# Kernel tuning notes

Measured on AMD Instinct MI355X. Metric: run time of the kernel, lower is better.

## Reference

```python
import jax, jax.numpy as jnp
import numpy as np

N = 100000      # nodes
E = 1600000     # edges (avg degree 16)
DIN = 32        # input feature dim
H = 16          # nhidden
DEPTH = 4       # number of SAGEConv layers


def setup_inputs() -> dict:
    key = jax.random.key(0)
    ks = jax.random.split(key, 16)
    s = 0.1
    inp = {
        "x": jax.random.normal(ks[0], (N, DIN), jnp.float32),
        "edge_index": jax.random.randint(ks[1], (2, E), 0, N, dtype=jnp.int64),
        # SAGEConv layer 0: in=DIN -> out=H. lin_l has bias, lin_r has no bias (PyG default).
        "Wl0": jax.random.normal(ks[2], (H, DIN), jnp.float32) * s,
        "bl0": jnp.zeros((H,), jnp.float32),
        "Wr0": jax.random.normal(ks[3], (H, DIN), jnp.float32) * s,
        # SAGEConv layers 1..3: in=H -> out=H, stacked.
        "Wls": jax.random.normal(ks[4], (DEPTH - 1, H, H), jnp.float32) * s,
        "bls": jnp.zeros((DEPTH - 1, H), jnp.float32),
        "Wrs": jax.random.normal(ks[5], (DEPTH - 1, H, H), jnp.float32) * s,
        # lin_out MLP: [H, 2H, 2H, 1] with acts [silu, silu, None], no batch norm.
        "W1": jax.random.normal(ks[6], (2 * H, H), jnp.float32) * s,
        "b1": jnp.zeros((2 * H,), jnp.float32),
        "W2": jax.random.normal(ks[7], (2 * H, 2 * H), jnp.float32) * s,
        "b2": jnp.zeros((2 * H,), jnp.float32),
        "W3": jax.random.normal(ks[8], (1, 2 * H), jnp.float32) * s,
        "b3": jnp.zeros((1,), jnp.float32),
    }
    return inp


def reference(x, edge_index, Wl0, bl0, Wr0, Wls, bls, Wrs, W1, b1, W2, b2, W3, b3):
    src = edge_index[0]  # message source (x_j)
    dst = edge_index[1]  # aggregation target (x_i)

    def sage(h, Wl, bl, Wr):
        # sum-aggregate neighbor features, then lin_l(agg) + lin_r(h)
        agg = jax.ops.segment_sum(h[src], dst, num_segments=N)  # [N, d]
        return agg @ Wl.T + bl + h @ Wr.T

    x = jax.nn.silu(sage(x, Wl0, bl0, Wr0))
    for i in range(DEPTH - 1):
        x = jax.nn.silu(sage(x, Wls[i], bls[i], Wrs[i]))

    out = jax.nn.silu(x @ W1.T + b1)
    out = jax.nn.silu(out @ W2.T + b2)
    out = out @ W3.T + b3  # [N, 1]
    return out
```

## Files before the change

kernel.cpp:

```cpp
#include <hip/hip_runtime.h>


#define SH     7
#define BWID   128
#define NBMAX  1024
#define CHUNK  4096
#define EPT    (CHUNK / 256)

__device__ __forceinline__ float silu_f(float v) {
    return v * __builtin_amdgcn_rcpf(1.0f + __expf(-v));
}

__device__ __forceinline__ float bf_lo(unsigned u) { return __uint_as_float(u << 16); }
__device__ __forceinline__ float bf_hi(unsigned u) { return __uint_as_float(u & 0xFFFF0000u); }
__device__ __forceinline__ unsigned short f2bf(float f) {
    unsigned x = __float_as_uint(f);
    unsigned r = x + 0x7FFFu + ((x >> 16) & 1u);
    return (unsigned short)(r >> 16);
}
__device__ __forceinline__ unsigned pack_bf2(float a, float b) {
    return (unsigned)f2bf(a) | ((unsigned)f2bf(b) << 16);
}


__global__ __launch_bounds__(256) void bucket_hist(
    const int* __restrict__ dst, int* __restrict__ bcnt, int ne)
{
    __shared__ int sh[NBMAX];
    const int t = threadIdx.x;
    for (int i = t; i < NBMAX; i += 256) sh[i] = 0;
    __syncthreads();
    const int base = blockIdx.x * CHUNK;
    for (int i = t; i < CHUNK; i += 256) {
        const int e = base + i;
        if (e < ne) atomicAdd(&sh[dst[e] >> SH], 1);
    }
    __syncthreads();
    for (int b = t; b < NBMAX; b += 256) {
        const int c = sh[b];
        if (c) atomicAdd(&bcnt[b], c);
    }
}

__global__ __launch_bounds__(1024) void bucket_scan(
    const int* __restrict__ bcnt, int* __restrict__ bbase,
    int* __restrict__ cursors, int* __restrict__ noff, int nbuck, int n, int ne)
{
    __shared__ int sh[NBMAX];
    const int t = threadIdx.x;
    const int c = (t < nbuck) ? bcnt[t] : 0;
    sh[t] = c;
    __syncthreads();
    int v = c;
    for (int off = 1; off < NBMAX; off <<= 1) {
        const int add = (t >= off) ? sh[t - off] : 0;
        __syncthreads();
        v += add;
        sh[t] = v;
        __syncthreads();
    }
    const int excl = v - c;
    if (t < nbuck) { bbase[t] = excl; cursors[t] = excl; }
    if (t == 0) { bbase[nbuck] = ne; noff[n] = ne; }
}

__global__ __launch_bounds__(256) void bin_kernel(
    const int* __restrict__ src, const int* __restrict__ dst,
    int* __restrict__ cursors, unsigned* __restrict__ binned0, int ne)
{
    __shared__ int   s_hist[NBMAX];
    __shared__ int   s_scan[NBMAX];
    __shared__ int   s_gbase[NBMAX];
    __shared__ int   s_p[256];
    __shared__ uint2 s_items[CHUNK];

    const int t = threadIdx.x;
    const int base = blockIdx.x * CHUNK;
    const int cnt = min(CHUNK, ne - base);

    int es[EPT], ed[EPT];
#pragma unroll
    for (int j = 0; j < EPT; ++j) {
        const int i = t + j * 256;
        if (i < cnt) { es[j] = src[base + i]; ed[j] = dst[base + i]; }
        else         { es[j] = -1; ed[j] = -1; }
    }

    for (int i = t; i < NBMAX; i += 256) s_hist[i] = 0;
    __syncthreads();
#pragma unroll
    for (int j = 0; j < EPT; ++j)
        if (es[j] >= 0) atomicAdd(&s_hist[ed[j] >> SH], 1);
    __syncthreads();

    const int l0 = s_hist[4 * t], l1 = s_hist[4 * t + 1];
    const int l2 = s_hist[4 * t + 2], l3 = s_hist[4 * t + 3];
    const int psum = l0 + l1 + l2 + l3;
    s_p[t] = psum;
    __syncthreads();
    int v = psum;
    for (int off = 1; off < 256; off <<= 1) {
        const int add = (t >= off) ? s_p[t - off] : 0;
        __syncthreads();
        v += add;
        s_p[t] = v;
        __syncthreads();
    }
    const int ex = v - psum;
    s_scan[4 * t] = ex;
    s_scan[4 * t + 1] = ex + l0;
    s_scan[4 * t + 2] = ex + l0 + l1;
    s_scan[4 * t + 3] = ex + l0 + l1 + l2;
    __syncthreads();

    for (int b = t; b < NBMAX; b += 256) {
        const int c = s_hist[b];
        s_gbase[b] = c ? atomicAdd(&cursors[b], c) : 0;
    }
    __syncthreads();
    for (int i = t; i < NBMAX; i += 256) s_hist[i] = 0;
    __syncthreads();

#pragma unroll
    for (int j = 0; j < EPT; ++j) {
        if (es[j] >= 0) {
            const int b  = ed[j] >> SH;
            const int ld = ed[j] & (BWID - 1);
            const int r  = atomicAdd(&s_hist[b], 1);
            s_items[s_scan[b] + r] = make_uint2((unsigned)b,
                                                ((unsigned)ld << 17) | (unsigned)es[j]);
        }
    }
    __syncthreads();

    for (int i = t; i < cnt; i += 256) {
        const uint2 it = s_items[i];
        const int b = (int)it.x;
        binned0[s_gbase[b] + (i - s_scan[b])] = it.y;
    }
}

__global__ __launch_bounds__(256) void node_sort(
    const unsigned* __restrict__ binned0, const int* __restrict__ bbase,
    int* __restrict__ binned1, int* __restrict__ noff, int n)
{
    __shared__ int cnt[BWID];
    __shared__ int off_[BWID];
    const int b = blockIdx.x, t = threadIdx.x;
    const int beg = bbase[b], end = bbase[b + 1];

    if (t < BWID) cnt[t] = 0;
    __syncthreads();
    for (int k = beg + t; k < end; k += 256)
        atomicAdd(&cnt[binned0[k] >> 17], 1);
    __syncthreads();

    if (t < BWID) off_[t] = cnt[t];
    __syncthreads();
    for (int o = 1; o < BWID; o <<= 1) {
        const int add = (t < BWID && t >= o) ? off_[t - o] : 0;
        __syncthreads();
        if (t < BWID) off_[t] += add;
        __syncthreads();
    }
    if (t < BWID) off_[t] -= cnt[t];
    __syncthreads();

    if (t < BWID) {
        const int node = (b << SH) + t;
        if (node <= n) noff[node] = beg + off_[t];
        cnt[t] = 0;
    }
    __syncthreads();

    for (int k = beg + t; k < end; k += 256) {
        const unsigned u = binned0[k];
        const int ld = (int)(u >> 17);
        const int r = atomicAdd(&cnt[ld], 1);
        binned1[beg + off_[ld] + r] = (int)(u & 0x1FFFFu);
    }
}


__device__ __forceinline__ void gather16(
    const int* __restrict__ binned1, const uint4* __restrict__ h4,
    int beg, int end, int q, float* p)
{
#pragma unroll
    for (int i = 0; i < 16; ++i) p[i] = 0.f;
    int k = beg + q;
    for (; k + 2 < end; k += 4) {
        const int s0 = binned1[k];
        const int s1 = binned1[k + 2];
        const uint4 a0 = h4[(size_t)s0 * 2];
        const uint4 a1 = h4[(size_t)s0 * 2 + 1];
        const uint4 b0 = h4[(size_t)s1 * 2];
        const uint4 b1 = h4[(size_t)s1 * 2 + 1];
        p[0] += bf_lo(a0.x); p[1] += bf_hi(a0.x); p[2] += bf_lo(a0.y); p[3] += bf_hi(a0.y);
        p[4] += bf_lo(a0.z); p[5] += bf_hi(a0.z); p[6] += bf_lo(a0.w); p[7] += bf_hi(a0.w);
        p[8] += bf_lo(a1.x); p[9] += bf_hi(a1.x); p[10]+= bf_lo(a1.y); p[11]+= bf_hi(a1.y);
        p[12]+= bf_lo(a1.z); p[13]+= bf_hi(a1.z); p[14]+= bf_lo(a1.w); p[15]+= bf_hi(a1.w);
        p[0] += bf_lo(b0.x); p[1] += bf_hi(b0.x); p[2] += bf_lo(b0.y); p[3] += bf_hi(b0.y);
        p[4] += bf_lo(b0.z); p[5] += bf_hi(b0.z); p[6] += bf_lo(b0.w); p[7] += bf_hi(b0.w);
        p[8] += bf_lo(b1.x); p[9] += bf_hi(b1.x); p[10]+= bf_lo(b1.y); p[11]+= bf_hi(b1.y);
        p[12]+= bf_lo(b1.z); p[13]+= bf_hi(b1.z); p[14]+= bf_lo(b1.w); p[15]+= bf_hi(b1.w);
    }
    if (k < end) {
        const int s0 = binned1[k];
        const uint4 a0 = h4[(size_t)s0 * 2];
        const uint4 a1 = h4[(size_t)s0 * 2 + 1];
        p[0] += bf_lo(a0.x); p[1] += bf_hi(a0.x); p[2] += bf_lo(a0.y); p[3] += bf_hi(a0.y);
        p[4] += bf_lo(a0.z); p[5] += bf_hi(a0.z); p[6] += bf_lo(a0.w); p[7] += bf_hi(a0.w);
        p[8] += bf_lo(a1.x); p[9] += bf_hi(a1.x); p[10]+= bf_lo(a1.y); p[11]+= bf_hi(a1.y);
        p[12]+= bf_lo(a1.z); p[13]+= bf_hi(a1.z); p[14]+= bf_lo(a1.w); p[15]+= bf_hi(a1.w);
    }
#pragma unroll
    for (int i = 0; i < 16; ++i) p[i] += __shfl_xor(p[i], 1);
}

__global__ __launch_bounds__(256) void fused_agg_dense(
    const int* __restrict__ noff, const int* __restrict__ binned1,
    const unsigned* __restrict__ hl_in,
    const float* __restrict__ acc_in,
    const float* __restrict__ Wl, const float* __restrict__ bl,
    const float* __restrict__ Wr,
    unsigned* __restrict__ hl_out,
    float* __restrict__ acc_out,
    int n)
{
    __shared__ float sWl[256], sWr[256], sbl[16];
    const int t = threadIdx.x;
    if (t < 256) { sWl[t] = Wl[t]; sWr[t] = Wr[t]; }
    if (t < 16) sbl[t] = bl[t];
    __syncthreads();

    const int node = (blockIdx.x << SH) + (t >> 1);
    if (node >= n) return;
    const int q = t & 1;
    const int beg = noff[node], end = noff[node + 1];

    float p[16];
    gather16(binned1, (const uint4*)hl_in, beg, end, q, p);

    const float4* __restrict__ ai = (const float4*)(acc_in + (size_t)node * 16);
    float h[16];
#pragma unroll
    for (int r = 0; r < 4; ++r) {
        const float4 a = ai[r];
        h[4*r+0] = silu_f(a.x + p[4*r+0]);
        h[4*r+1] = silu_f(a.y + p[4*r+1]);
        h[4*r+2] = silu_f(a.z + p[4*r+2]);
        h[4*r+3] = silu_f(a.w + p[4*r+3]);
    }

    const float4* __restrict__ sWl4 = (const float4*)sWl;
    const float4* __restrict__ sWr4 = (const float4*)sWr;
    float ol[8], oa[8];
#pragma unroll
    for (int jj = 0; jj < 8; ++jj) {
        const int j = 8 * q + jj;
        float al = 0.f, ar = 0.f;
#pragma unroll
        for (int d4 = 0; d4 < 4; ++d4) {
            const float4 wl = sWl4[j * 4 + d4];
            const float4 wr = sWr4[j * 4 + d4];
            al = fmaf(wl.x, h[4*d4+0], al); al = fmaf(wl.y, h[4*d4+1], al);
            al = fmaf(wl.z, h[4*d4+2], al); al = fmaf(wl.w, h[4*d4+3], al);
            ar = fmaf(wr.x, h[4*d4+0], ar); ar = fmaf(wr.y, h[4*d4+1], ar);
            ar = fmaf(wr.z, h[4*d4+2], ar); ar = fmaf(wr.w, h[4*d4+3], ar);
        }
        ol[jj] = al;
        oa[jj] = sbl[j] + ar;
    }

    ((uint4*)hl_out)[(size_t)node * 2 + q] =
        make_uint4(pack_bf2(ol[0], ol[1]), pack_bf2(ol[2], ol[3]),
                   pack_bf2(ol[4], ol[5]), pack_bf2(ol[6], ol[7]));
    float4* __restrict__ ap = (float4*)(acc_out + (size_t)node * 16);
    ap[2 * q]     = make_float4(oa[0], oa[1], oa[2], oa[3]);
    ap[2 * q + 1] = make_float4(oa[4], oa[5], oa[6], oa[7]);
}

__global__ __launch_bounds__(256) void fused_agg_mlp(
    const int* __restrict__ noff, const int* __restrict__ binned1,
    const unsigned* __restrict__ hl_in, const float* __restrict__ acc_in,
    const float* __restrict__ W1, const float* __restrict__ b1,
    const float* __restrict__ W2, const float* __restrict__ b2,
    const float* __restrict__ W3, const float* __restrict__ b3,
    float* __restrict__ out, int n)
{
    __shared__ float sW1[512], sW2[1024], sb1[32], sb2[32], sW3[32];
    __shared__ float sb3;
    const int t = threadIdx.x;
    for (int i = t; i < 512; i += 256) sW1[i] = W1[i];
    for (int i = t; i < 1024; i += 256) sW2[i] = W2[i];
    if (t < 32) { sb1[t] = b1[t]; sb2[t] = b2[t]; sW3[t] = W3[t]; }
    if (t == 0) sb3 = b3[0];
    __syncthreads();

    const int node = (blockIdx.x << SH) + (t >> 1);
    if (node >= n) return;
    const int q = t & 1;
    const int beg = noff[node], end = noff[node + 1];

    float p[16];
    gather16(binned1, (const uint4*)hl_in, beg, end, q, p);

    const float4* __restrict__ ai = (const float4*)(acc_in + (size_t)node * 16);
    float h[16];
#pragma unroll
    for (int r = 0; r < 4; ++r) {
        const float4 a = ai[r];
        h[4*r+0] = silu_f(a.x + p[4*r+0]);
        h[4*r+1] = silu_f(a.y + p[4*r+1]);
        h[4*r+2] = silu_f(a.z + p[4*r+2]);
        h[4*r+3] = silu_f(a.w + p[4*r+3]);
    }

    const float4* __restrict__ sW1v = (const float4*)sW1;
    float a1[16];
#pragma unroll
    for (int jj = 0; jj < 16; ++jj) {
        const int j = 16 * q + jj;
        float s = sb1[j];
#pragma unroll
        for (int d4 = 0; d4 < 4; ++d4) {
            const float4 w = sW1v[j * 4 + d4];
            s = fmaf(w.x, h[4*d4+0], s); s = fmaf(w.y, h[4*d4+1], s);
            s = fmaf(w.z, h[4*d4+2], s); s = fmaf(w.w, h[4*d4+3], s);
        }
        a1[jj] = silu_f(s);
    }

    float A1[32];
#pragma unroll
    for (int i = 0; i < 16; ++i) {
        const float mine  = a1[i];
        const float other = __shfl_xor(mine, 1);
        A1[i]      = q ? other : mine;
        A1[16 + i] = q ? mine  : other;
    }

    const float4* __restrict__ sW2v = (const float4*)sW2;
    float part = 0.f;
#pragma unroll
    for (int jj = 0; jj < 16; ++jj) {
        const int j = 16 * q + jj;
        float s = sb2[j];
#pragma unroll
        for (int d4 = 0; d4 < 8; ++d4) {
            const float4 w = sW2v[j * 8 + d4];
            s = fmaf(w.x, A1[4*d4+0], s); s = fmaf(w.y, A1[4*d4+1], s);
            s = fmaf(w.z, A1[4*d4+2], s); s = fmaf(w.w, A1[4*d4+3], s);
        }
        part = fmaf(sW3[j], silu_f(s), part);
    }
    part += __shfl_xor(part, 1);
    if (q == 0) out[node] = part + sb3;
}

__global__ __launch_bounds__(128) void dense0(
    const float* __restrict__ x,
    const float* __restrict__ Wl, const float* __restrict__ bl,
    const float* __restrict__ Wr,
    unsigned* __restrict__ hlb, float* __restrict__ acc, int n)
{
    __shared__ float sWl[512], sWr[512], sbl[16];
    const int t = threadIdx.x;
    for (int i = t; i < 512; i += 128) { sWl[i] = Wl[i]; sWr[i] = Wr[i]; }
    if (t < 16) sbl[t] = bl[t];
    __syncthreads();

    const int node = blockIdx.x * 128 + t;
    if (node >= n) return;

    float h[32];
    const float4* __restrict__ xp = (const float4*)(x + (size_t)node * 32);
#pragma unroll
    for (int r = 0; r < 8; ++r) {
        const float4 v = xp[r];
        h[4*r+0] = v.x; h[4*r+1] = v.y; h[4*r+2] = v.z; h[4*r+3] = v.w;
    }

    const float4* __restrict__ sWl4 = (const float4*)sWl;
    const float4* __restrict__ sWr4 = (const float4*)sWr;
    float ol[16], oa[16];
#pragma unroll
    for (int j = 0; j < 16; ++j) {
        float al = 0.f, ar = 0.f;
#pragma unroll
        for (int d4 = 0; d4 < 8; ++d4) {
            const float4 wl = sWl4[j * 8 + d4];
            const float4 wr = sWr4[j * 8 + d4];
            al = fmaf(wl.x, h[4*d4+0], al); al = fmaf(wl.y, h[4*d4+1], al);
            al = fmaf(wl.z, h[4*d4+2], al); al = fmaf(wl.w, h[4*d4+3], al);
            ar = fmaf(wr.x, h[4*d4+0], ar); ar = fmaf(wr.y, h[4*d4+1], ar);
            ar = fmaf(wr.z, h[4*d4+2], ar); ar = fmaf(wr.w, h[4*d4+3], ar);
        }
        ol[j] = al;
        oa[j] = sbl[j] + ar;
    }

    unsigned u[8];
#pragma unroll
    for (int r = 0; r < 8; ++r) u[r] = pack_bf2(ol[2*r], ol[2*r+1]);
    uint4* __restrict__ hp = (uint4*)(hlb + (size_t)node * 8);
    hp[0] = make_uint4(u[0], u[1], u[2], u[3]);
    hp[1] = make_uint4(u[4], u[5], u[6], u[7]);
    float4* __restrict__ ap = (float4*)(acc + (size_t)node * 16);
#pragma unroll
    for (int r = 0; r < 4; ++r)
        ap[r] = make_float4(oa[4*r], oa[4*r+1], oa[4*r+2], oa[4*r+3]);
}

extern "C" void kernel_launch(void* const* d_in, const int* in_sizes, int n_in,
                              void* d_out, int out_size, void* d_ws, size_t ws_size,
                              hipStream_t stream)
{
    const float* x   = (const float*)d_in[0];
    const int*   ei  = (const int*)d_in[1];
    const float* Wl0 = (const float*)d_in[2];
    const float* bl0 = (const float*)d_in[3];
    const float* Wr0 = (const float*)d_in[4];
    const float* Wls = (const float*)d_in[5];
    const float* bls = (const float*)d_in[6];
    const float* Wrs = (const float*)d_in[7];
    const float* W1  = (const float*)d_in[8];
    const float* b1  = (const float*)d_in[9];
    const float* W2  = (const float*)d_in[10];
    const float* b2  = (const float*)d_in[11];
    const float* W3  = (const float*)d_in[12];
    const float* b3  = (const float*)d_in[13];

    const int n  = in_sizes[0] / 32;
    const int ne = in_sizes[1] / 2;
    const int* src = ei;
    const int* dst = ei + ne;
    const int nbuck = (n + BWID - 1) >> SH;

    float*    acc0    = (float*)d_ws;
    float*    acc1    = acc0 + (size_t)n * 16;
    unsigned* hlbA    = (unsigned*)(acc1 + (size_t)n * 16);
    unsigned* hlbB    = hlbA + (size_t)n * 8;
    int*      binned1 = (int*)(hlbB + (size_t)n * 8);
    int*      noff    = binned1 + (size_t)ne;
    int*      bcnt    = noff + (n + 1);
    int*      bbase   = bcnt + NBMAX;
    int*      cursors = bbase + NBMAX + 1;
    unsigned* binned0 = (unsigned*)(cursors + NBMAX);

    const int nb = (n + 127) / 128;
    const int cb = (ne + CHUNK - 1) / CHUNK;

    hipMemsetAsync(bcnt, 0, NBMAX * sizeof(int), stream);
    bucket_hist<<<cb, 256, 0, stream>>>(dst, bcnt, ne);
    bucket_scan<<<1, 1024, 0, stream>>>(bcnt, bbase, cursors, noff, nbuck, n, ne);
    bin_kernel<<<cb, 256, 0, stream>>>(src, dst, cursors, binned0, ne);
    node_sort<<<nbuck, 256, 0, stream>>>(binned0, bbase, binned1, noff, n);

    dense0<<<nb, 128, 0, stream>>>(x, Wl0, bl0, Wr0, hlbA, acc0, n);
    fused_agg_dense<<<nbuck, 256, 0, stream>>>(noff, binned1, hlbA, acc0,
        Wls + 0,   bls + 0,  Wrs + 0,   hlbB, acc1, n);
    fused_agg_dense<<<nbuck, 256, 0, stream>>>(noff, binned1, hlbB, acc1,
        Wls + 256, bls + 16, Wrs + 256, hlbA, acc0, n);
    fused_agg_dense<<<nbuck, 256, 0, stream>>>(noff, binned1, hlbA, acc0,
        Wls + 512, bls + 32, Wrs + 512, hlbB, acc1, n);
    fused_agg_mlp<<<nbuck, 256, 0, stream>>>(noff, binned1, hlbB, acc1,
        W1, b1, W2, b2, W3, b3, (float*)d_out, n);
}
```

Before: 177.8 us.

## Fuse layer-0 dense into binning kernel and use four lanes per node in gather

The standalone dense0 kernel is removed. Its per-node 32-to-16 projection now runs at the tail of the edge-binning kernel, with each of its 256-thread blocks handling 256 nodes, which saves one launch. The aggregation kernels (fused_agg_dense and fused_agg_mlp) now assign four lanes per node instead of two. They use a stride-4 neighbour gather, two xor-shuffle reductions, a split of the output columns across the four lanes and added occupancy hints. The aim is more memory-level parallelism in the gather, in exchange for extra shuffles. Node coverage in the fused bin kernel now depends on the edge-chunk block count times 256 being at least the node count.

```diff
diff --git a/kernel.cpp b/kernel.cpp
--- a/kernel.cpp
+++ b/kernel.cpp
@@ -64,17 +64,25 @@
     if (t == 0) { bbase[nbuck] = ne; noff[n] = ne; }
 }
 
-__global__ __launch_bounds__(256) void bin_kernel(
+__global__ __launch_bounds__(256) void bin_dense0(
     const int* __restrict__ src, const int* __restrict__ dst,
-    int* __restrict__ cursors, unsigned* __restrict__ binned0, int ne)
+    int* __restrict__ cursors, unsigned* __restrict__ binned0,
+    const float* __restrict__ x,
+    const float* __restrict__ Wl0, const float* __restrict__ bl0,
+    const float* __restrict__ Wr0,
+    unsigned* __restrict__ hlb, float* __restrict__ acc, int n, int ne)
 {
     __shared__ int   s_hist[NBMAX];
     __shared__ int   s_scan[NBMAX];
     __shared__ int   s_gbase[NBMAX];
     __shared__ int   s_p[256];
     __shared__ uint2 s_items[CHUNK];
+    __shared__ float sWl[512], sWr[512], sbl[16];
 
     const int t = threadIdx.x;
+    for (int i = t; i < 512; i += 256) { sWl[i] = Wl0[i]; sWr[i] = Wr0[i]; }
+    if (t < 16) sbl[t] = bl0[t];
+
     const int base = blockIdx.x * CHUNK;
     const int cnt = min(CHUNK, ne - base);
 
@@ -138,6 +146,47 @@
         const int b = (int)it.x;
         binned0[s_gbase[b] + (i - s_scan[b])] = it.y;
     }
+
+    const int node = blockIdx.x * 256 + t;
+    if (node >= n) return;
+
+    float h[32];
+    const float4* __restrict__ xp = (const float4*)(x + (size_t)node * 32);
+#pragma unroll
+    for (int r = 0; r < 8; ++r) {
+        const float4 vv = xp[r];
+        h[4*r+0] = vv.x; h[4*r+1] = vv.y; h[4*r+2] = vv.z; h[4*r+3] = vv.w;
+    }
+
+    const float4* __restrict__ sWl4 = (const float4*)sWl;
+    const float4* __restrict__ sWr4 = (const float4*)sWr;
+    float ol[16], oa[16];
+#pragma unroll
+    for (int j = 0; j < 16; ++j) {
+        float al = 0.f, ar = 0.f;
+#pragma unroll
+        for (int d4 = 0; d4 < 8; ++d4) {
+            const float4 wl = sWl4[j * 8 + d4];
+            const float4 wr = sWr4[j * 8 + d4];
+            al = fmaf(wl.x, h[4*d4+0], al); al = fmaf(wl.y, h[4*d4+1], al);
+            al = fmaf(wl.z, h[4*d4+2], al); al = fmaf(wl.w, h[4*d4+3], al);
+            ar = fmaf(wr.x, h[4*d4+0], ar); ar = fmaf(wr.y, h[4*d4+1], ar);
+            ar = fmaf(wr.z, h[4*d4+2], ar); ar = fmaf(wr.w, h[4*d4+3], ar);
+        }
+        ol[j] = al;
+        oa[j] = sbl[j] + ar;
+    }
+
+    unsigned u[8];
+#pragma unroll
+    for (int r = 0; r < 8; ++r) u[r] = pack_bf2(ol[2*r], ol[2*r+1]);
+    uint4* __restrict__ hp = (uint4*)(hlb + (size_t)node * 8);
+    hp[0] = make_uint4(u[0], u[1], u[2], u[3]);
+    hp[1] = make_uint4(u[4], u[5], u[6], u[7]);
+    float4* __restrict__ ap = (float4*)(acc + (size_t)node * 16);
+#pragma unroll
+    for (int r = 0; r < 4; ++r)
+        ap[r] = make_float4(oa[4*r], oa[4*r+1], oa[4*r+2], oa[4*r+3]);
 }
 
 __global__ __launch_bounds__(256) void node_sort(
@@ -182,16 +231,16 @@
 }
 
 
-__device__ __forceinline__ void gather16(
+__device__ __forceinline__ void gather16_4(
     const int* __restrict__ binned1, const uint4* __restrict__ h4,
     int beg, int end, int q, float* p)
 {
 #pragma unroll
     for (int i = 0; i < 16; ++i) p[i] = 0.f;
     int k = beg + q;
-    for (; k + 2 < end; k += 4) {
+    for (; k + 4 < end; k += 8) {
         const int s0 = binned1[k];
-        const int s1 = binned1[k + 2];
+        const int s1 = binned1[k + 4];
         const uint4 a0 = h4[(size_t)s0 * 2];
         const uint4 a1 = h4[(size_t)s0 * 2 + 1];
         const uint4 b0 = h4[(size_t)s1 * 2];
@@ -216,31 +265,31 @@
     }
 #pragma unroll
     for (int i = 0; i < 16; ++i) p[i] += __shfl_xor(p[i], 1);
-}
-
-__global__ __launch_bounds__(256) void fused_agg_dense(
+#pragma unroll
+    for (int i = 0; i < 16; ++i) p[i] += __shfl_xor(p[i], 2);
+}
+
+__global__ __launch_bounds__(256, 4) void fused_agg_dense(
     const int* __restrict__ noff, const int* __restrict__ binned1,
-    const unsigned* __restrict__ hl_in,
-    const float* __restrict__ acc_in,
+    const unsigned* __restrict__ hl_in, const float* __restrict__ acc_in,
     const float* __restrict__ Wl, const float* __restrict__ bl,
     const float* __restrict__ Wr,
-    unsigned* __restrict__ hl_out,
-    float* __restrict__ acc_out,
-    int n)
+    unsigned* __restrict__ hl_out, float* __restrict__ acc_out, int n)
 {
     __shared__ float sWl[256], sWr[256], sbl[16];
     const int t = threadIdx.x;
-    if (t < 256) { sWl[t] = Wl[t]; sWr[t] = Wr[t]; }
+    sWl[t] = Wl[t]; sWr[t] = Wr[t];
     if (t < 16) sbl[t] = bl[t];
     __syncthreads();
 
-    const int node = (blockIdx.x << SH) + (t >> 1);
+    const int gid = blockIdx.x * 256 + t;
+    const int node = gid >> 2;
     if (node >= n) return;
-    const int q = t & 1;
+    const int q = t & 3;
     const int beg = noff[node], end = noff[node + 1];
 
     float p[16];
-    gather16(binned1, (const uint4*)hl_in, beg, end, q, p);
+    gather16_4(binned1, (const uint4*)hl_in, beg, end, q, p);
 
     const float4* __restrict__ ai = (const float4*)(acc_in + (size_t)node * 16);
     float h[16];
@@ -255,10 +304,10 @@
 
     const float4* __restrict__ sWl4 = (const float4*)sWl;
     const float4* __restrict__ sWr4 = (const float4*)sWr;
-    float ol[8], oa[8];
-#pragma unroll
-    for (int jj = 0; jj < 8; ++jj) {
-        const int j = 8 * q + jj;
+    float ol[4], oa[4];
+#pragma unroll
+    for (int jj = 0; jj < 4; ++jj) {
+        const int j = 4 * q + jj;
         float al = 0.f, ar = 0.f;
 #pragma unroll
         for (int d4 = 0; d4 < 4; ++d4) {
@@ -273,15 +322,13 @@
         oa[jj] = sbl[j] + ar;
     }
 
-    ((uint4*)hl_out)[(size_t)node * 2 + q] =
-        make_uint4(pack_bf2(ol[0], ol[1]), pack_bf2(ol[2], ol[3]),
-                   pack_bf2(ol[4], ol[5]), pack_bf2(ol[6], ol[7]));
-    float4* __restrict__ ap = (float4*)(acc_out + (size_t)node * 16);
-    ap[2 * q]     = make_float4(oa[0], oa[1], oa[2], oa[3]);
-    ap[2 * q + 1] = make_float4(oa[4], oa[5], oa[6], oa[7]);
-}
-
-__global__ __launch_bounds__(256) void fused_agg_mlp(
+    ((uint2*)hl_out)[(size_t)node * 4 + q] =
+        make_uint2(pack_bf2(ol[0], ol[1]), pack_bf2(ol[2], ol[3]));
+    ((float4*)acc_out)[(size_t)node * 4 + q] =
+        make_float4(oa[0], oa[1], oa[2], oa[3]);
+}
+
+__global__ __launch_bounds__(256, 3) void fused_agg_mlp(
     const int* __restrict__ noff, const int* __restrict__ binned1,
     const unsigned* __restrict__ hl_in, const float* __restrict__ acc_in,
     const float* __restrict__ W1, const float* __restrict__ b1,
@@ -298,13 +345,14 @@
     if (t == 0) sb3 = b3[0];
     __syncthreads();
 
-    const int node = (blockIdx.x << SH) + (t >> 1);
+    const int gid = blockIdx.x * 256 + t;
+    const int node = gid >> 2;
     if (node >= n) return;
-    const int q = t & 1;
+    const int q = t & 3;
     const int beg = noff[node], end = noff[node + 1];
 
     float p[16];
-    gather16(binned1, (const uint4*)hl_in, beg, end, q, p);
+    gather16_4(binned1, (const uint4*)hl_in, beg, end, q, p);
 
     const float4* __restrict__ ai = (const float4*)(acc_in + (size_t)node * 16);
     float h[16];
@@ -318,10 +366,10 @@
     }
 
     const float4* __restrict__ sW1v = (const float4*)sW1;
-    float a1[16];
-#pragma unroll
-    for (int jj = 0; jj < 16; ++jj) {
-        const int j = 16 * q + jj;
+    float a1[8];
+#pragma unroll
+    for (int jj = 0; jj < 8; ++jj) {
+        const int j = 8 * q + jj;
         float s = sb1[j];
 #pragma unroll
         for (int d4 = 0; d4 < 4; ++d4) {
@@ -332,20 +380,30 @@
         a1[jj] = silu_f(s);
     }
 
-    float A1[32];
-#pragma unroll
-    for (int i = 0; i < 16; ++i) {
+    float t0[16];
+#pragma unroll
+    for (int i = 0; i < 8; ++i) {
         const float mine  = a1[i];
         const float other = __shfl_xor(mine, 1);
-        A1[i]      = q ? other : mine;
-        A1[16 + i] = q ? mine  : other;
+        const bool hi = (q & 1);
+        t0[i]     = hi ? other : mine;
+        t0[8 + i] = hi ? mine  : other;
+    }
+    float A1[32];
+#pragma unroll
+    for (int i = 0; i < 16; ++i) {
+        const float mine  = t0[i];
+        const float other = __shfl_xor(mine, 2);
+        const bool hi = (q & 2);
+        A1[i]      = hi ? other : mine;
+        A1[16 + i] = hi ? mine  : other;
     }
 
     const float4* __restrict__ sW2v = (const float4*)sW2;
     float part = 0.f;
 #pragma unroll
-    for (int jj = 0; jj < 16; ++jj) {
-        const int j = 16 * q + jj;
+    for (int jj = 0; jj < 8; ++jj) {
+        const int j = 8 * q + jj;
         float s = sb2[j];
 #pragma unroll
         for (int d4 = 0; d4 < 8; ++d4) {
@@ -356,61 +414,8 @@
         part = fmaf(sW3[j], silu_f(s), part);
     }
     part += __shfl_xor(part, 1);
+    part += __shfl_xor(part, 2);
     if (q == 0) out[node] = part + sb3;
-}
-
-__global__ __launch_bounds__(128) void dense0(
-    const float* __restrict__ x,
-    const float* __restrict__ Wl, const float* __restrict__ bl,
-    const float* __restrict__ Wr,
-    unsigned* __restrict__ hlb, float* __restrict__ acc, int n)
-{
-    __shared__ float sWl[512], sWr[512], sbl[16];
-    const int t = threadIdx.x;
-    for (int i = t; i < 512; i += 128) { sWl[i] = Wl[i]; sWr[i] = Wr[i]; }
-    if (t < 16) sbl[t] = bl[t];
-    __syncthreads();
-
-    const int node = blockIdx.x * 128 + t;
-    if (node >= n) return;
-
-    float h[32];
-    const float4* __restrict__ xp = (const float4*)(x + (size_t)node * 32);
-#pragma unroll
-    for (int r = 0; r < 8; ++r) {
-        const float4 v = xp[r];
-        h[4*r+0] = v.x; h[4*r+1] = v.y; h[4*r+2] = v.z; h[4*r+3] = v.w;
-    }
-
-    const float4* __restrict__ sWl4 = (const float4*)sWl;
-    const float4* __restrict__ sWr4 = (const float4*)sWr;
-    float ol[16], oa[16];
-#pragma unroll
-    for (int j = 0; j < 16; ++j) {
-        float al = 0.f, ar = 0.f;
-#pragma unroll
-        for (int d4 = 0; d4 < 8; ++d4) {
-            const float4 wl = sWl4[j * 8 + d4];
-            const float4 wr = sWr4[j * 8 + d4];
-            al = fmaf(wl.x, h[4*d4+0], al); al = fmaf(wl.y, h[4*d4+1], al);
-            al = fmaf(wl.z, h[4*d4+2], al); al = fmaf(wl.w, h[4*d4+3], al);
-            ar = fmaf(wr.x, h[4*d4+0], ar); ar = fmaf(wr.y, h[4*d4+1], ar);
-            ar = fmaf(wr.z, h[4*d4+2], ar); ar = fmaf(wr.w, h[4*d4+3], ar);
-        }
-        ol[j] = al;
-        oa[j] = sbl[j] + ar;
-    }
-
-    unsigned u[8];
-#pragma unroll
-    for (int r = 0; r < 8; ++r) u[r] = pack_bf2(ol[2*r], ol[2*r+1]);
-    uint4* __restrict__ hp = (uint4*)(hlb + (size_t)node * 8);
-    hp[0] = make_uint4(u[0], u[1], u[2], u[3]);
-    hp[1] = make_uint4(u[4], u[5], u[6], u[7]);
-    float4* __restrict__ ap = (float4*)(acc + (size_t)node * 16);
-#pragma unroll
-    for (int r = 0; r < 4; ++r)
-        ap[r] = make_float4(oa[4*r], oa[4*r+1], oa[4*r+2], oa[4*r+3]);
 }
 
 extern "C" void kernel_launch(void* const* d_in, const int* in_sizes, int n_in,
@@ -449,22 +454,22 @@
     int*      cursors = bbase + NBMAX + 1;
     unsigned* binned0 = (unsigned*)(cursors + NBMAX);
 
-    const int nb = (n + 127) / 128;
     const int cb = (ne + CHUNK - 1) / CHUNK;
+    const int lb = (n * 4 + 255) / 256;
 
     hipMemsetAsync(bcnt, 0, NBMAX * sizeof(int), stream);
     bucket_hist<<<cb, 256, 0, stream>>>(dst, bcnt, ne);
     bucket_scan<<<1, 1024, 0, stream>>>(bcnt, bbase, cursors, noff, nbuck, n, ne);
-    bin_kernel<<<cb, 256, 0, stream>>>(src, dst, cursors, binned0, ne);
+    bin_dense0<<<cb, 256, 0, stream>>>(src, dst, cursors, binned0,
+                                       x, Wl0, bl0, Wr0, hlbA, acc0, n, ne);
     node_sort<<<nbuck, 256, 0, stream>>>(binned0, bbase, binned1, noff, n);
 
-    dense0<<<nb, 128, 0, stream>>>(x, Wl0, bl0, Wr0, hlbA, acc0, n);
-    fused_agg_dense<<<nbuck, 256, 0, stream>>>(noff, binned1, hlbA, acc0,
+    fused_agg_dense<<<lb, 256, 0, stream>>>(noff, binned1, hlbA, acc0,
         Wls + 0,   bls + 0,  Wrs + 0,   hlbB, acc1, n);
-    fused_agg_dense<<<nbuck, 256, 0, stream>>>(noff, binned1, hlbB, acc1,
+    fused_agg_dense<<<lb, 256, 0, stream>>>(noff, binned1, hlbB, acc1,
         Wls + 256, bls + 16, Wrs + 256, hlbA, acc0, n);
-    fused_agg_dense<<<nbuck, 256, 0, stream>>>(noff, binned1, hlbA, acc0,
+    fused_agg_dense<<<lb, 256, 0, stream>>>(noff, binned1, hlbA, acc0,
         Wls + 512, bls + 32, Wrs + 512, hlbB, acc1, n);
-    fused_agg_mlp<<<nbuck, 256, 0, stream>>>(noff, binned1, hlbB, acc1,
+    fused_agg_mlp<<<lb, 256, 0, stream>>>(noff, binned1, hlbB, acc1,
         W1, b1, W2, b2, W3, b3, (float*)d_out, n);
 }
```

Result: no change. 179.1 us (+0.7%).
